# Performance work log

Hardware: AMD Instinct MI355X
Metric: run time of the kernel (lower is better)

Reference implementation:

```python
import jax, jax.numpy as jnp
import numpy as np
import math

FIRE_THRESH = 0.85
SQRT_2_OVER_PI = math.sqrt(2.0 / math.pi)

def _gelu(x):
    # tanh-approx GELU, exactly as in the torch module
    return 0.5 * x * (1.0 + jnp.tanh(SQRT_2_OVER_PI * (x + 0.044715 * x * x * x)))

def setup_inputs() -> dict:
    key = jax.random.key(0)
    ks = jax.random.split(key, 8)
    B, T, D, N = 8, 4096, 1024, 512
    x = jax.random.normal(ks[0], (B, T, D), dtype=jnp.float32)
    log_beta = jnp.asarray(math.log(10.0), dtype=jnp.float32)
    log_k_inject = jnp.asarray(math.log(0.1), dtype=jnp.float32)
    # buffer keys are stored L2-normalized in the original module
    raw_keys = jax.random.normal(ks[1], (N, D), dtype=jnp.float32)
    buf_keys = raw_keys / jnp.maximum(jnp.linalg.norm(raw_keys, axis=-1, keepdims=True), 1e-12)
    buf_vals = jax.random.normal(ks[2], (N, D), dtype=jnp.float32)
    global_sum = jax.random.normal(ks[3], (D,), dtype=jnp.float32)
    mask = jnp.ones((N,), dtype=bool)
    hit_count = jax.random.randint(ks[4], (N,), 0, 100, dtype=jnp.int64 if jax.config.jax_enable_x64 else jnp.int32)
    n_global = 300
    return {"x": x, "log_beta": log_beta, "log_k_inject": log_k_inject,
            "buf_keys": buf_keys, "buf_vals": buf_vals, "global_sum": global_sum,
            "mask": mask, "hit_count": hit_count, "n_global": n_global}

def reference(x, log_beta, log_k_inject, buf_keys, buf_vals, global_sum, mask, hit_count, n_global):
    B, T, D = x.shape
    y = _gelu(x)  # [B,T,D]
    # m_curr = mean over all tokens, detached in the original
    m_curr = jax.lax.stop_gradient(jnp.mean(y.reshape(-1, D), axis=0))  # [D]
    beta = jnp.clip(jnp.exp(log_beta), 1.0, 50.0)
    k_inject = jnp.clip(jnp.exp(log_k_inject), 0.001, 2.0)
    # retrieval (no_grad block in torch)
    q = m_curr / jnp.maximum(jnp.linalg.norm(m_curr), 1e-12)  # [D]
    sims = buf_keys @ q                                        # [N]
    logits = jnp.where(mask, beta * sims, -1e9)
    attn = jax.nn.softmax(logits, axis=0)
    retrieved = attn @ buf_vals                                # [D]
    nearest_idx = jnp.argmax(logits)
    sims_plain = jnp.where(mask, sims, -1.0)
    hit = hit_count[nearest_idx] + (sims_plain[nearest_idx] > FIRE_THRESH).astype(hit_count.dtype)
    t = k_inject * jnp.log(hit.astype(x.dtype) + 1.0)
    global_mean = global_sum / max(int(n_global), 1)
    delta = jax.lax.stop_gradient(retrieved - global_mean)     # [D]
    return y + t * delta.reshape(1, 1, D)
```

## Files before the change

kernel.cpp:

```cpp
#include <hip/hip_runtime.h>
#include <math.h>

#define ROWS 32768
#define D    1024
#define DF4  256
#define NKEYS 512
#define CSB  512
#define CSR  64
#define R1B  16
#define SIMB 16
#define RETB 8

typedef float f32x4 __attribute__((ext_vector_type(4)));

__device__ __forceinline__ float gelu1(float x) {
    float z = 0.7978845608028654f * fmaf(0.044715f * x, x * x, x);
    float e = __expf(2.0f * z);
    return x - x / (e + 1.0f);
}

__global__ __launch_bounds__(256) void k_colsum(const float4* __restrict__ x4,
                                                float4* __restrict__ partial4) {
    int t = threadIdx.x, b = blockIdx.x;
    const float4* p = x4 + (size_t)b * CSR * DF4 + t;
    float4 acc = make_float4(0.f, 0.f, 0.f, 0.f);
#pragma unroll 8
    for (int r = 0; r < CSR; ++r) {
        float4 v = p[(size_t)r * DF4];
        acc.x += gelu1(v.x); acc.y += gelu1(v.y);
        acc.z += gelu1(v.z); acc.w += gelu1(v.w);
    }
    partial4[(size_t)b * DF4 + t] = acc;
}

__global__ __launch_bounds__(1024) void k_red1(const float* __restrict__ partial,
                                               float* __restrict__ partial2) {
    int d = threadIdx.x, b = blockIdx.x;
    float s = 0.f;
#pragma unroll
    for (int p = 0; p < 32; ++p) s += partial[(size_t)(b * 32 + p) * D + d];
    partial2[b * D + d] = s;
}

__global__ __launch_bounds__(256) void k_sims(const float4* __restrict__ partial2_4,
                                              const float4* __restrict__ keys4,
                                              float* __restrict__ sims,
                                              float* __restrict__ n2out) {
    int t = threadIdx.x, b = blockIdx.x;
    int wave = t >> 6, lane = t & 63;
    float4 m4 = make_float4(0.f, 0.f, 0.f, 0.f);
#pragma unroll
    for (int p = 0; p < R1B; ++p) {
        float4 v = partial2_4[p * DF4 + t];
        m4.x += v.x; m4.y += v.y; m4.z += v.z; m4.w += v.w;
    }
    m4.x *= (1.0f/32768.0f); m4.y *= (1.0f/32768.0f);
    m4.z *= (1.0f/32768.0f); m4.w *= (1.0f/32768.0f);

    __shared__ float wsum[4];
    if (b == 0) {
        float d2 = m4.x*m4.x + m4.y*m4.y + m4.z*m4.z + m4.w*m4.w;
#pragma unroll
        for (int off = 32; off > 0; off >>= 1) d2 += __shfl_down(d2, off, 64);
        if (lane == 0) wsum[wave] = d2;
        __syncthreads();
        if (t == 0) n2out[0] = wsum[0] + wsum[1] + wsum[2] + wsum[3];
        __syncthreads();
    }
    for (int j = 0; j < 32; ++j) {
        int n = b * 32 + j;
        float4 k = keys4[(size_t)n * DF4 + t];
        float d = k.x*m4.x + k.y*m4.y + k.z*m4.z + k.w*m4.w;
#pragma unroll
        for (int off = 32; off > 0; off >>= 1) d += __shfl_down(d, off, 64);
        if (lane == 0) wsum[wave] = d;
        __syncthreads();
        if (t == 0) sims[n] = wsum[0] + wsum[1] + wsum[2] + wsum[3];
        __syncthreads();
    }
}

__global__ __launch_bounds__(256) void k_ret(const float* __restrict__ sims,
                                             const float* __restrict__ n2in,
                                             const float4* __restrict__ vals4,
                                             const float* __restrict__ log_beta,
                                             const float* __restrict__ log_kinj,
                                             const int* __restrict__ hit_count,
                                             float* __restrict__ tval,
                                             float4* __restrict__ rp4) {
    int t = threadIdx.x, b = blockIdx.x;
    float beta = fminf(fmaxf(__expf(log_beta[0]), 1.0f), 50.0f);
    float inv_norm = 1.0f / fmaxf(sqrtf(n2in[0]), 1e-12f);
    float s0 = sims[t], s1 = sims[t + 256];
    float l0 = beta * (s0 * inv_norm), l1 = beta * (s1 * inv_norm);

    __shared__ float red[256];
    float mv = fmaxf(l0, l1);
    red[t] = mv;
    __syncthreads();
    for (int st = 128; st > 0; st >>= 1) {
        if (t < st) red[t] = fmaxf(red[t], red[t + st]);
        __syncthreads();
    }
    float lmax = red[0];
    __syncthreads();
    float e0 = __expf(l0 - lmax), e1 = __expf(l1 - lmax);
    red[t] = e0 + e1;
    __syncthreads();
    for (int st = 128; st > 0; st >>= 1) {
        if (t < st) red[t] += red[t + st];
        __syncthreads();
    }
    float inv_sum = 1.0f / red[0];
    __shared__ float w[NKEYS];
    w[t] = e0 * inv_sum;
    w[t + 256] = e1 * inv_sum;
    __syncthreads();

    if (b == 0) {
        __shared__ float amv[256];
        __shared__ int   ami[256];
        float v; int i;
        if (l1 > l0) { v = l1; i = t + 256; } else { v = l0; i = t; }
        amv[t] = v; ami[t] = i;
        __syncthreads();
        for (int st = 128; st > 0; st >>= 1) {
            if (t < st) {
                float ov = amv[t + st]; int oi = ami[t + st];
                if (ov > amv[t] || (ov == amv[t] && oi < ami[t])) { amv[t] = ov; ami[t] = oi; }
            }
            __syncthreads();
        }
        if (t == 0) {
            int nearest = ami[0];
            float sp = sims[nearest] * inv_norm;
            int hit = hit_count[nearest] + (sp > 0.85f ? 1 : 0);
            float kinj = fminf(fmaxf(__expf(log_kinj[0]), 0.001f), 2.0f);
            tval[0] = kinj * logf((float)hit + 1.0f);
        }
    }

    float4 acc = make_float4(0.f, 0.f, 0.f, 0.f);
#pragma unroll 8
    for (int j = 0; j < 64; ++j) {
        int n = b * 64 + j;
        float a = w[n];
        float4 v = vals4[(size_t)n * DF4 + t];
        acc.x = fmaf(a, v.x, acc.x); acc.y = fmaf(a, v.y, acc.y);
        acc.z = fmaf(a, v.z, acc.z); acc.w = fmaf(a, v.w, acc.w);
    }
    rp4[(size_t)b * DF4 + t] = acc;
}

__global__ __launch_bounds__(256) void k_out(const float4* __restrict__ x4,
                                             const float4* __restrict__ rp4,
                                             const float4* __restrict__ gsum4,
                                             const int* __restrict__ ngl,
                                             const float* __restrict__ tval,
                                             f32x4* __restrict__ out4) {
    const int NF4 = ROWS * DF4;
    int i0 = blockIdx.x * 256 + threadIdx.x;
    int stride = gridDim.x * 256;
    int c = i0 & (DF4 - 1);

    float rx = 0.f, ry = 0.f, rz = 0.f, rw = 0.f;
#pragma unroll
    for (int bb = 0; bb < RETB; ++bb) {
        float4 v = rp4[bb * DF4 + c];
        rx += v.x; ry += v.y; rz += v.z; rw += v.w;
    }
    int ng = ngl[0];
    float invn = 1.0f / (float)(ng > 1 ? ng : 1);
    float tv = tval[0];
    float4 g = gsum4[c];
    float ax = tv * (rx - g.x * invn);
    float ay = tv * (ry - g.y * invn);
    float az = tv * (rz - g.z * invn);
    float aw = tv * (rw - g.w * invn);

    for (int i = i0; i < NF4; i += stride) {
        float4 v = x4[i];
        f32x4 o;
        o.x = gelu1(v.x) + ax;
        o.y = gelu1(v.y) + ay;
        o.z = gelu1(v.z) + az;
        o.w = gelu1(v.w) + aw;
        __builtin_nontemporal_store(o, &out4[i]);
    }
}

extern "C" void kernel_launch(void* const* d_in, const int* in_sizes, int n_in,
                              void* d_out, int out_size, void* d_ws, size_t ws_size,
                              hipStream_t stream) {
    const float* x          = (const float*)d_in[0];
    const float* log_beta   = (const float*)d_in[1];
    const float* log_kinj   = (const float*)d_in[2];
    const float* buf_keys   = (const float*)d_in[3];
    const float* buf_vals   = (const float*)d_in[4];
    const float* global_sum = (const float*)d_in[5];
    const int*   hit_count  = (const int*)d_in[7];
    const int*   n_global   = (const int*)d_in[8];
    float* out = (float*)d_out;

    float* ws = (float*)d_ws;
    float* partial  = ws;
    float* partial2 = partial + (size_t)CSB * D;
    float* sims     = partial2 + R1B * D;
    float* n2       = sims + NKEYS;
    float* tval     = n2 + 4;
    float* rp       = tval + 4;

    k_colsum<<<CSB, 256, 0, stream>>>((const float4*)x, (float4*)partial);
    k_red1 <<<R1B, 1024, 0, stream>>>(partial, partial2);
    k_sims <<<SIMB, 256, 0, stream>>>((const float4*)partial2, (const float4*)buf_keys,
                                      sims, n2);
    k_ret  <<<RETB, 256, 0, stream>>>(sims, n2, (const float4*)buf_vals,
                                      log_beta, log_kinj, hit_count, tval, (float4*)rp);
    k_out  <<<4096, 256, 0, stream>>>((const float4*)x, (const float4*)rp,
                                      (const float4*)global_sum, n_global, tval,
                                      (f32x4*)out);
}
```

Baseline: 99.61 us.

## Split query normalization into own kernel, widen sims grid, use plain stores

Adds a single-block kernel that reduces the column partials, computes the normalized query vector and writes it out. The similarity kernel then runs one block per key instead of sixteen blocks looping over 32 keys each, and softmax no longer rescales by the norm. The output kernel drops nontemporal stores for ordinary stores and halves its grid. This adds one launch and changes the cache behaviour of the large output write.

```diff
diff --git a/kernel.cpp b/kernel.cpp
--- a/kernel.cpp
+++ b/kernel.cpp
@@ -8,10 +8,7 @@
 #define CSB  512
 #define CSR  64
 #define R1B  16
-#define SIMB 16
 #define RETB 8
-
-typedef float f32x4 __attribute__((ext_vector_type(4)));
 
 __device__ __forceinline__ float gelu1(float x) {
     float z = 0.7978845608028654f * fmaf(0.044715f * x, x * x, x);
@@ -42,46 +39,41 @@
     partial2[b * D + d] = s;
 }
 
-__global__ __launch_bounds__(256) void k_sims(const float4* __restrict__ partial2_4,
-                                              const float4* __restrict__ keys4,
-                                              float* __restrict__ sims,
-                                              float* __restrict__ n2out) {
-    int t = threadIdx.x, b = blockIdx.x;
+__global__ __launch_bounds__(1024) void k_q(const float* __restrict__ partial2,
+                                            float* __restrict__ q) {
+    __shared__ float red[1024];
+    int d = threadIdx.x;
+    float s = 0.f;
+#pragma unroll
+    for (int p = 0; p < R1B; ++p) s += partial2[p * D + d];
+    float m = s * (1.0f / 32768.0f);
+    red[d] = m * m;
+    __syncthreads();
+    for (int st = 512; st > 0; st >>= 1) {
+        if (d < st) red[d] += red[d + st];
+        __syncthreads();
+    }
+    float inv = 1.0f / fmaxf(sqrtf(red[0]), 1e-12f);
+    q[d] = m * inv;
+}
+
+__global__ __launch_bounds__(256) void k_sims(const float4* __restrict__ keys4,
+                                              const float4* __restrict__ q4,
+                                              float* __restrict__ sims) {
+    int n = blockIdx.x, t = threadIdx.x;
+    float4 k = keys4[(size_t)n * DF4 + t];
+    float4 qq = q4[t];
+    float v = k.x * qq.x + k.y * qq.y + k.z * qq.z + k.w * qq.w;
+#pragma unroll
+    for (int off = 32; off > 0; off >>= 1) v += __shfl_down(v, off, 64);
+    __shared__ float wsum[4];
     int wave = t >> 6, lane = t & 63;
-    float4 m4 = make_float4(0.f, 0.f, 0.f, 0.f);
-#pragma unroll
-    for (int p = 0; p < R1B; ++p) {
-        float4 v = partial2_4[p * DF4 + t];
-        m4.x += v.x; m4.y += v.y; m4.z += v.z; m4.w += v.w;
-    }
-    m4.x *= (1.0f/32768.0f); m4.y *= (1.0f/32768.0f);
-    m4.z *= (1.0f/32768.0f); m4.w *= (1.0f/32768.0f);
-
-    __shared__ float wsum[4];
-    if (b == 0) {
-        float d2 = m4.x*m4.x + m4.y*m4.y + m4.z*m4.z + m4.w*m4.w;
-#pragma unroll
-        for (int off = 32; off > 0; off >>= 1) d2 += __shfl_down(d2, off, 64);
-        if (lane == 0) wsum[wave] = d2;
-        __syncthreads();
-        if (t == 0) n2out[0] = wsum[0] + wsum[1] + wsum[2] + wsum[3];
-        __syncthreads();
-    }
-    for (int j = 0; j < 32; ++j) {
-        int n = b * 32 + j;
-        float4 k = keys4[(size_t)n * DF4 + t];
-        float d = k.x*m4.x + k.y*m4.y + k.z*m4.z + k.w*m4.w;
-#pragma unroll
-        for (int off = 32; off > 0; off >>= 1) d += __shfl_down(d, off, 64);
-        if (lane == 0) wsum[wave] = d;
-        __syncthreads();
-        if (t == 0) sims[n] = wsum[0] + wsum[1] + wsum[2] + wsum[3];
-        __syncthreads();
-    }
+    if (lane == 0) wsum[wave] = v;
+    __syncthreads();
+    if (t == 0) sims[n] = wsum[0] + wsum[1] + wsum[2] + wsum[3];
 }
 
 __global__ __launch_bounds__(256) void k_ret(const float* __restrict__ sims,
-                                             const float* __restrict__ n2in,
                                              const float4* __restrict__ vals4,
                                              const float* __restrict__ log_beta,
                                              const float* __restrict__ log_kinj,
@@ -90,13 +82,11 @@
                                              float4* __restrict__ rp4) {
     int t = threadIdx.x, b = blockIdx.x;
     float beta = fminf(fmaxf(__expf(log_beta[0]), 1.0f), 50.0f);
-    float inv_norm = 1.0f / fmaxf(sqrtf(n2in[0]), 1e-12f);
     float s0 = sims[t], s1 = sims[t + 256];
-    float l0 = beta * (s0 * inv_norm), l1 = beta * (s1 * inv_norm);
+    float l0 = beta * s0, l1 = beta * s1;
 
     __shared__ float red[256];
-    float mv = fmaxf(l0, l1);
-    red[t] = mv;
+    red[t] = fmaxf(l0, l1);
     __syncthreads();
     for (int st = 128; st > 0; st >>= 1) {
         if (t < st) red[t] = fmaxf(red[t], red[t + st]);
@@ -133,7 +123,7 @@
         }
         if (t == 0) {
             int nearest = ami[0];
-            float sp = sims[nearest] * inv_norm;
+            float sp = sims[nearest];
             int hit = hit_count[nearest] + (sp > 0.85f ? 1 : 0);
             float kinj = fminf(fmaxf(__expf(log_kinj[0]), 0.001f), 2.0f);
             tval[0] = kinj * logf((float)hit + 1.0f);
@@ -157,7 +147,7 @@
                                              const float4* __restrict__ gsum4,
                                              const int* __restrict__ ngl,
                                              const float* __restrict__ tval,
-                                             f32x4* __restrict__ out4) {
+                                             float4* __restrict__ out4) {
     const int NF4 = ROWS * DF4;
     int i0 = blockIdx.x * 256 + threadIdx.x;
     int stride = gridDim.x * 256;
@@ -180,12 +170,12 @@
 
     for (int i = i0; i < NF4; i += stride) {
         float4 v = x4[i];
-        f32x4 o;
+        float4 o;
         o.x = gelu1(v.x) + ax;
         o.y = gelu1(v.y) + ay;
         o.z = gelu1(v.z) + az;
         o.w = gelu1(v.w) + aw;
-        __builtin_nontemporal_store(o, &out4[i]);
+        out4[i] = o;
     }
 }
 
@@ -205,18 +195,18 @@
     float* ws = (float*)d_ws;
     float* partial  = ws;
     float* partial2 = partial + (size_t)CSB * D;
-    float* sims     = partial2 + R1B * D;
-    float* n2       = sims + NKEYS;
-    float* tval     = n2 + 4;
+    float* q        = partial2 + R1B * D;
+    float* sims     = q + D;
+    float* tval     = sims + NKEYS;
     float* rp       = tval + 4;
 
     k_colsum<<<CSB, 256, 0, stream>>>((const float4*)x, (float4*)partial);
     k_red1 <<<R1B, 1024, 0, stream>>>(partial, partial2);
-    k_sims <<<SIMB, 256, 0, stream>>>((const float4*)partial2, (const float4*)buf_keys,
-                                      sims, n2);
-    k_ret  <<<RETB, 256, 0, stream>>>(sims, n2, (const float4*)buf_vals,
+    k_q    <<<1, 1024, 0, stream>>>(partial2, q);
+    k_sims <<<NKEYS, 256, 0, stream>>>((const float4*)buf_keys, (const float4*)q, sims);
+    k_ret  <<<RETB, 256, 0, stream>>>(sims, (const float4*)buf_vals,
                                       log_beta, log_kinj, hit_count, tval, (float4*)rp);
-    k_out  <<<4096, 256, 0, stream>>>((const float4*)x, (const float4*)rp,
+    k_out  <<<2048, 256, 0, stream>>>((const float4*)x, (const float4*)rp,
                                       (const float4*)global_sum, n_global, tval,
-                                      (f32x4*)out);
-}
+                                      (float4*)out);
+}
```

Result: faster. 90.77 us (-8.9%).
